# Optimization experiments

Hardware: AMD Instinct MI355X
Metric: run time of the kernel (lower is better)

## Reference

```python
import jax, jax.numpy as jnp
import numpy as np
import math

B, T, C, H = 2, 2048, 1024, 16
D = C // H  # head dim = 64

def setup_inputs() -> dict:
    key = jax.random.key(0)
    ks = jax.random.split(key, 5)
    scale_in = 1.0 / math.sqrt(C)
    x = jax.random.normal(ks[0], (B, T, C), dtype=jnp.float32)
    W_attn = jax.random.normal(ks[1], (C, 3 * C), dtype=jnp.float32) * scale_in
    b_attn = jnp.zeros((3 * C,), dtype=jnp.float32)
    W_proj = jax.random.normal(ks[2], (C, C), dtype=jnp.float32) * scale_in
    b_proj = jnp.zeros((C,), dtype=jnp.float32)
    return {"x": x, "W_attn": W_attn, "b_attn": b_attn, "W_proj": W_proj, "b_proj": b_proj}

def reference(x, W_attn, b_attn, W_proj, b_proj):
    qkv = x @ W_attn + b_attn                      # [B,T,3C]
    q, k, v = jnp.split(qkv, 3, axis=2)            # each [B,T,C]
    def heads(t):
        return t.reshape(B, T, H, D).transpose(0, 2, 1, 3)  # [B,H,T,D]
    q, k, v = heads(q), heads(k), heads(v)
    # NOTE: original scales by 1/sqrt(n_embd), not 1/sqrt(head_dim)
    scores = jnp.einsum('bhtd,bhsd->bhts', q, k) / math.sqrt(C)  # [B,H,T,T]
    mask = jnp.tril(jnp.ones((T, T), dtype=scores.dtype))
    scores = scores + (mask - 1.0) * 1e9
    attn = jax.nn.softmax(scores, axis=-1)
    out = jnp.einsum('bhts,bhsd->bhtd', attn, v)   # [B,H,T,D]
    out = out.transpose(0, 2, 1, 3).reshape(B, T, C)
    return out @ W_proj + b_proj
```

## Files before the change

kernel.cpp:

```cpp
#include <hip/hip_runtime.h>
#include <hip/hip_bf16.h>


typedef __attribute__((ext_vector_type(8))) short bf16x8;
typedef __attribute__((ext_vector_type(4))) short bf16x4;
typedef __attribute__((ext_vector_type(4))) float f32x4;

__device__ __forceinline__ short f2bs(float f) {
    union { __hip_bfloat16 h; short s; } u;
    u.h = __float2bfloat16(f);
    return u.s;
}

__device__ __forceinline__ short f2bs_trunc(float f) {
    return (short)(__float_as_uint(f) >> 16);
}

#define GLOAD_LDS16(gp, lp)                                                        \
    __builtin_amdgcn_global_load_lds((const __attribute__((address_space(1))) void*)(gp), \
                                     (__attribute__((address_space(3))) void*)(lp), 16, 0, 0)

__global__ __launch_bounds__(256) void convx(
    const float* __restrict__ X, short* __restrict__ Xb)
{
    const size_t i = ((size_t)blockIdx.x * 256 + threadIdx.x) * 8;
    float4 a = *(const float4*)(X + i);
    float4 b = *(const float4*)(X + i + 4);
    bf16x8 s;
    s[0] = f2bs(a.x); s[1] = f2bs(a.y); s[2] = f2bs(a.z); s[3] = f2bs(a.w);
    s[4] = f2bs(b.x); s[5] = f2bs(b.y); s[6] = f2bs(b.z); s[7] = f2bs(b.w);
    *(bf16x8*)(Xb + i) = s;
}

__global__ __launch_bounds__(256) void convt(
    const float* __restrict__ W, short* __restrict__ Wt, int K, int N)
{
    __shared__ short t[64 * 72];
    const int tid = threadIdx.x;
    const int n0 = blockIdx.x * 64, k0 = blockIdx.y * 64;
    #pragma unroll
    for (int i = 0; i < 4; i++) {
        int k = (tid >> 4) + i * 16;
        int n = (tid & 15) * 4;
        float4 v = *(const float4*)(W + (size_t)(k0 + k) * N + n0 + n);
        t[(n + 0) * 72 + k] = f2bs(v.x);
        t[(n + 1) * 72 + k] = f2bs(v.y);
        t[(n + 2) * 72 + k] = f2bs(v.z);
        t[(n + 3) * 72 + k] = f2bs(v.w);
    }
    __syncthreads();
    #pragma unroll
    for (int i = 0; i < 2; i++) {
        int n  = (tid >> 3) + i * 32;
        int kc = (tid & 7) * 8;
        bf16x8 v = *(const bf16x8*)&t[n * 72 + kc];
        *(bf16x8*)(Wt + (size_t)(n0 + n) * K + k0 + kc) = v;
    }
}

__global__ __launch_bounds__(512) void qkv_gemm(
    const short* __restrict__ Xb, const short* __restrict__ Wt,
    const float* __restrict__ bias,
    short* __restrict__ Qw, short* __restrict__ Kw, short* __restrict__ Vt)
{
    __shared__ short LB[40960];

    const int tid  = threadIdx.x;
    const int lane = tid & 63;
    const int wid  = tid >> 6;
    const int wm = wid >> 2, wn = wid & 3;
    const int g = lane >> 4, cc = lane & 15;
    const int sw = cc & 7;

    const int bid   = blockIdx.x;
    const int xcd   = bid & 7;
    const int r     = bid >> 3;
    const int m0 = ((xcd & 3) * 8 + (r & 7)) * 128;
    const int n0 = ((xcd >> 2) * 8 + (r >> 3)) * 192;

    f32x4 acc[4][3];
    const f32x4 z4 = {0.f, 0.f, 0.f, 0.f};
    #pragma unroll
    for (int i = 0; i < 4; i++)
        #pragma unroll
        for (int j = 0; j < 3; j++) acc[i][j] = z4;

    auto STAGE = [&](int t, int buf) {
        const int k0 = t * 64;
        short* Ab = LB + buf * 8192;
        short* Bb = LB + 16384 + buf * 12288;
        #pragma unroll
        for (int j = 0; j < 2; j++) {
            int c = j * 512 + tid;
            int row = c >> 3, sch = (c & 7) ^ (row & 7);
            GLOAD_LDS16(Xb + (size_t)(m0 + row) * 1024 + k0 + sch * 8, Ab + c * 8);
        }
        #pragma unroll
        for (int j = 0; j < 3; j++) {
            int c = j * 512 + tid;
            int row = c >> 3, sch = (c & 7) ^ (row & 7);
            GLOAD_LDS16(Wt + (size_t)(n0 + row) * 1024 + k0 + sch * 8, Bb + c * 8);
        }
    };

    STAGE(0, 0);
    STAGE(1, 1);
    asm volatile("s_waitcnt vmcnt(5)" ::: "memory");
    asm volatile("s_barrier" ::: "memory");

    const int NT = 16;
    for (int t = 0; t < NT; t++) {
        const short* Ab = LB + (t & 1) * 8192;
        const short* Bb = LB + 16384 + (t & 1) * 12288;

        bf16x8 bfr[3][2];
        #pragma unroll
        for (int nf = 0; nf < 3; nf++)
            #pragma unroll
            for (int kk = 0; kk < 2; kk++)
                bfr[nf][kk] = *(const bf16x8*)&Bb[(wn * 48 + nf * 16 + cc) * 64 +
                                                  ((kk * 4 + g) ^ sw) * 8];
        bf16x8 af[4][2];
        #pragma unroll
        for (int mf = 0; mf < 4; mf++)
            #pragma unroll
            for (int kk = 0; kk < 2; kk++)
                af[mf][kk] = *(const bf16x8*)&Ab[(wm * 64 + mf * 16 + cc) * 64 +
                                                 ((kk * 4 + g) ^ sw) * 8];
        __builtin_amdgcn_s_setprio(1);
        #pragma unroll
        for (int mf = 0; mf < 4; mf++)
            #pragma unroll
            for (int nf = 0; nf < 3; nf++)
                #pragma unroll
                for (int kk = 0; kk < 2; kk++)
                    acc[mf][nf] = __builtin_amdgcn_mfma_f32_16x16x32_bf16(
                        af[mf][kk], bfr[nf][kk], acc[mf][nf], 0, 0, 0);
        __builtin_amdgcn_s_setprio(0);

        asm volatile("s_barrier" ::: "memory");
        if (t + 2 < NT) {
            STAGE(t + 2, t & 1);
            asm volatile("s_waitcnt vmcnt(5)" ::: "memory");
            asm volatile("s_barrier" ::: "memory");
        } else if (t + 1 < NT) {
            asm volatile("s_waitcnt vmcnt(0)" ::: "memory");
            asm volatile("s_barrier" ::: "memory");
        }
    }

    const float QSCALE = 0.04508422976f;
    const int vs = (n0 > 2048) ? n0 : 2048;
    const int nV = n0 + 192 - vs;
    short* Vstage = LB;

    __syncthreads();

    #pragma unroll
    for (int nf = 0; nf < 3; nf++) {
        int col = n0 + wn * 48 + nf * 16 + cc;
        int which = col >> 10;
        int ci = col & 1023;
        int h = ci >> 6, d = ci & 63;
        float bv = bias[col];
        #pragma unroll
        for (int mf = 0; mf < 4; mf++) {
            if (which == 2) {
                int tl = wm * 64 + mf * 16 + g * 4;
                int pl = (tl & ~31) | (((tl >> 2) & 3) * 8 + ((tl >> 4) & 1) * 4);
                bf16x4 pk;
                #pragma unroll
                for (int r2 = 0; r2 < 4; r2++) pk[r2] = f2bs(acc[mf][nf][r2] + bv);
                *(bf16x4*)&Vstage[(col - vs) * 136 + pl] = pk;
            } else {
                #pragma unroll
                for (int r2 = 0; r2 < 4; r2++) {
                    int row = m0 + wm * 64 + mf * 16 + g * 4 + r2;
                    int b = row >> 11, tt = row & 2047;
                    int bh = b * 16 + h;
                    float v = acc[mf][nf][r2] + bv;
                    if (which == 0) Qw[((size_t)bh * 2048 + tt) * 64 + d] = f2bs(v * QSCALE);
                    else            Kw[((size_t)bh * 2048 + tt) * 64 + d] = f2bs(v);
                }
            }
        }
    }

    if (nV > 0) {
        __syncthreads();
        const int bb = m0 >> 11;
        const int tbase = m0 & 2047;
        const int total = nV * 16;
        for (int cidx = tid; cidx < total; cidx += 512) {
            int vc = cidx >> 4, toff = (cidx & 15) * 8;
            bf16x8 v = *(const bf16x8*)&Vstage[vc * 136 + toff];
            int col = vs + vc;
            int ci = col & 1023;
            int h2 = ci >> 6, d2 = ci & 63;
            *(bf16x8*)(Vt + ((size_t)(bb * 16 + h2) * 64 + d2) * 2048 + tbase + toff) = v;
        }
    }
}

__global__ __launch_bounds__(256) void attn_v16(
    const short* __restrict__ Qw, const short* __restrict__ Kw,
    const short* __restrict__ Vt, short* __restrict__ Aout)
{
    __shared__ short Klds[2][64 * 64];
    __shared__ short Vlds[2][64 * 64];
    const int tid  = threadIdx.x;
    const int lane = tid & 63;
    const int wid  = tid >> 6;
    const int g = lane >> 4, cc = lane & 15;
    const int bid = blockIdx.x;
    const int bh = bid & 31;
    const int grp = 31 - (bid >> 5);
    const int b = bh >> 4, h = bh & 15;
    const short* Qb = Qw + (size_t)bh * 2048 * 64;
    const short* Kb = Kw + (size_t)bh * 2048 * 64;
    const short* Vb = Vt + (size_t)bh * 64 * 2048;

    const f32x4 z4 = {0.f, 0.f, 0.f, 0.f};
    bf16x8 ones;
    #pragma unroll
    for (int i = 0; i < 8; i++) ones[i] = (short)0x3F80;

    auto STAGE = [&](int t, int buf) {
        const int kv0 = t * 64;
        #pragma unroll
        for (int j = 0; j < 2; j++) {
            int c = tid + j * 256;
            int row = c >> 3, sch = (c & 7) ^ (row & 7);
            GLOAD_LDS16(Kb + (size_t)(kv0 + row) * 64 + sch * 8, &Klds[buf][c * 8]);
            GLOAD_LDS16(Vb + (size_t)row * 2048 + kv0 + sch * 8, &Vlds[buf][c * 8]);
        }
    };

    const int q0 = grp * 64 + wid * 16;
    const int NT = grp + 1;

    bf16x8 qf0[2];
    #pragma unroll
    for (int ds = 0; ds < 2; ds++)
        qf0[ds] = *(const bf16x8*)(Qb + (q0 + cc) * 64 + ds * 32 + g * 8);

    f32x4 o[4], ol;
    #pragma unroll
    for (int ch = 0; ch < 4; ch++) o[ch] = z4;
    ol = z4;
    float m_r = -1e30f;

    STAGE(0, 0);
    STAGE((NT > 1) ? 1 : 0, 1);
    asm volatile("s_waitcnt vmcnt(4)" ::: "memory");
    asm volatile("s_barrier" ::: "memory");

    for (int t = 0; t < NT; t++) {
        const int kv0 = t * 64;
        const short* Kt = Klds[t & 1];
        const short* Vt_ = Vlds[t & 1];
        const bool masked = (t == NT - 1);

        bf16x8 kf[8];
        #pragma unroll
        for (int kvc = 0; kvc < 4; kvc++) {
            int row = kvc * 16 + cc;
            #pragma unroll
            for (int ds = 0; ds < 2; ds++)
                kf[kvc * 2 + ds] = *(const bf16x8*)&Kt[row * 64 +
                                                       (((ds * 4 + g) ^ (row & 7)) * 8)];
        }
        f32x4 s_[4];
        #pragma unroll
        for (int kvc = 0; kvc < 4; kvc++) {
            s_[kvc] = z4;
            #pragma unroll
            for (int ds = 0; ds < 2; ds++)
                s_[kvc] = __builtin_amdgcn_mfma_f32_16x16x32_bf16(
                    kf[kvc * 2 + ds], qf0[ds], s_[kvc], 0, 0, 0);
        }
        bf16x8 vf[8];
        #pragma unroll
        for (int kvh = 0; kvh < 2; kvh++)
            #pragma unroll
            for (int ch = 0; ch < 4; ch++) {
                int row = ch * 16 + cc;
                vf[kvh * 4 + ch] = *(const bf16x8*)&Vt_[row * 64 +
                                                        (((kvh * 4 + g) ^ (row & 7)) * 8)];
            }

        bf16x8 pb_[2];
        {
            float sv[16];
            #pragma unroll
            for (int kvc = 0; kvc < 4; kvc++)
                #pragma unroll
                for (int r = 0; r < 4; r++) {
                    float v = s_[kvc][r];
                    if (masked) {
                        int kv = kv0 + kvc * 16 + g * 4 + r;
                        v = (kv <= q0 + cc) ? v : -1e30f;
                    }
                    sv[kvc * 4 + r] = v;
                }
            float lm = sv[0];
            #pragma unroll
            for (int i = 1; i < 16; i++) lm = fmaxf(lm, sv[i]);
            if (__any(lm > m_r + 6.0f)) {
                float mx = fmaxf(lm, __shfl_xor(lm, 16));
                mx = fmaxf(mx, __shfl_xor(mx, 32));
                float mn = fmaxf(m_r, mx);
                float a = exp2f(m_r - mn);
                #pragma unroll
                for (int ch = 0; ch < 4; ch++)
                    #pragma unroll
                    for (int r = 0; r < 4; r++) o[ch][r] *= a;
                #pragma unroll
                for (int r = 0; r < 4; r++) ol[r] *= a;
                m_r = mn;
            }
            #pragma unroll
            for (int i = 0; i < 16; i++) {
                float p = exp2f(sv[i] - m_r);
                pb_[i >> 3][i & 7] = f2bs_trunc(p);
            }
        }
        #pragma unroll
        for (int kvh = 0; kvh < 2; kvh++) {
            #pragma unroll
            for (int ch = 0; ch < 4; ch++)
                o[ch] = __builtin_amdgcn_mfma_f32_16x16x32_bf16(
                    vf[kvh * 4 + ch], pb_[kvh], o[ch], 0, 0, 0);
            ol = __builtin_amdgcn_mfma_f32_16x16x32_bf16(ones, pb_[kvh], ol, 0, 0, 0);
        }

        asm volatile("s_barrier" ::: "memory");
        if (t + 2 < NT) {
            STAGE(t + 2, t & 1);
            asm volatile("s_waitcnt vmcnt(4)" ::: "memory");
            asm volatile("s_barrier" ::: "memory");
        } else if (t + 1 < NT) {
            asm volatile("s_waitcnt vmcnt(0)" ::: "memory");
            asm volatile("s_barrier" ::: "memory");
        }
    }

    const float rl = 1.0f / ol[0];
    const int t2 = q0 + cc;
    #pragma unroll
    for (int ch = 0; ch < 4; ch++) {
        bf16x4 ov;
        #pragma unroll
        for (int r = 0; r < 4; r++) ov[r] = f2bs(o[ch][r] * rl);
        *(bf16x4*)(Aout + ((size_t)b * 2048 + t2) * 1024 + h * 64 + ch * 16 + g * 4) = ov;
    }
}

__global__ __launch_bounds__(512) void proj_gemm(
    const short* __restrict__ A, const short* __restrict__ Wt,
    const float* __restrict__ bias, float* __restrict__ Out)
{
    __shared__ short Alds[2][256 * 64];
    __shared__ short Blds[2][64 * 64];
    const int tid  = threadIdx.x;
    const int lane = tid & 63;
    const int wid  = tid >> 6;
    const int wm = wid >> 1, wn = wid & 1;
    const int g = lane >> 4, cc = lane & 15;
    const int sw = cc & 7;

    const int bid  = blockIdx.x;
    const int wgid = (bid & 7) * 32 + (bid >> 3);
    const int n0 = (wgid >> 4) * 64;
    const int m0 = (wgid & 15) * 256;

    f32x4 acc[4][2];
    const f32x4 z4 = {0.f, 0.f, 0.f, 0.f};
    #pragma unroll
    for (int i = 0; i < 4; i++)
        #pragma unroll
        for (int j = 0; j < 2; j++) acc[i][j] = z4;

    auto STAGE = [&](int t, int buf) {
        const int k0 = t * 64;
        #pragma unroll
        for (int j = 0; j < 4; j++) {
            int c = j * 512 + wid * 64 + lane;
            int row = c >> 3, sch = (c & 7) ^ (row & 7);
            GLOAD_LDS16(A + (size_t)(m0 + row) * 1024 + k0 + sch * 8,
                        &Alds[buf][c * 8]);
        }
        {
            int c = wid * 64 + lane;
            int row = c >> 3, sch = (c & 7) ^ (row & 7);
            GLOAD_LDS16(Wt + (size_t)(n0 + row) * 1024 + k0 + sch * 8,
                        &Blds[buf][c * 8]);
        }
    };

    STAGE(0, 0);
    STAGE(1, 1);
    asm volatile("s_waitcnt vmcnt(5)" ::: "memory");
    asm volatile("s_barrier" ::: "memory");

    const int NT = 16;
    for (int t = 0; t < NT; t++) {
        const short* Ab = Alds[t & 1];
        const short* Bb = Blds[t & 1];

        bf16x8 bfr[2][2];
        #pragma unroll
        for (int nf = 0; nf < 2; nf++)
            #pragma unroll
            for (int kk = 0; kk < 2; kk++)
                bfr[nf][kk] = *(const bf16x8*)&Bb[(wn * 32 + nf * 16 + cc) * 64 +
                                                  ((kk * 4 + g) ^ sw) * 8];
        bf16x8 af[4][2];
        #pragma unroll
        for (int mf = 0; mf < 4; mf++)
            #pragma unroll
            for (int kk = 0; kk < 2; kk++)
                af[mf][kk] = *(const bf16x8*)&Ab[(wm * 64 + mf * 16 + cc) * 64 +
                                                 ((kk * 4 + g) ^ sw) * 8];
        __builtin_amdgcn_s_setprio(1);
        #pragma unroll
        for (int mf = 0; mf < 4; mf++)
            #pragma unroll
            for (int nf = 0; nf < 2; nf++)
                #pragma unroll
                for (int kk = 0; kk < 2; kk++)
                    acc[mf][nf] = __builtin_amdgcn_mfma_f32_16x16x32_bf16(
                        af[mf][kk], bfr[nf][kk], acc[mf][nf], 0, 0, 0);
        __builtin_amdgcn_s_setprio(0);

        asm volatile("s_barrier" ::: "memory");
        if (t + 2 < NT) {
            STAGE(t + 2, t & 1);
            asm volatile("s_waitcnt vmcnt(5)" ::: "memory");
            asm volatile("s_barrier" ::: "memory");
        } else if (t + 1 < NT) {
            asm volatile("s_waitcnt vmcnt(0)" ::: "memory");
            asm volatile("s_barrier" ::: "memory");
        }
    }

    #pragma unroll
    for (int nf = 0; nf < 2; nf++) {
        int col = n0 + wn * 32 + nf * 16 + cc;
        float bv = bias[col];
        #pragma unroll
        for (int mf = 0; mf < 4; mf++) {
            #pragma unroll
            for (int r = 0; r < 4; r++) {
                int row = m0 + wm * 64 + mf * 16 + g * 4 + r;
                Out[(size_t)row * 1024 + col] = acc[mf][nf][r] + bv;
            }
        }
    }
}

extern "C" void kernel_launch(void* const* d_in, const int* in_sizes, int n_in,
                              void* d_out, int out_size, void* d_ws, size_t ws_size,
                              hipStream_t stream)
{
    const float* x      = (const float*)d_in[0];
    const float* W_attn = (const float*)d_in[1];
    const float* b_attn = (const float*)d_in[2];
    const float* W_proj = (const float*)d_in[3];
    const float* b_proj = (const float*)d_in[4];
    float* out = (float*)d_out;

    const size_t SZ = (size_t)4096 * 1024;
    short* R1 = (short*)d_ws;
    short* Qw = R1 + SZ;
    short* Kw = Qw + SZ;
    short* Vt = Kw + SZ;

    short* Wt_attn = R1;
    short* Aout    = R1;
    short* Wt_proj = Qw;
    short* Xb      = (short*)d_out;

    convx<<<dim3(2048), 256, 0, stream>>>(x, Xb);
    convt<<<dim3(48, 16), 256, 0, stream>>>(W_attn, Wt_attn, 1024, 3072);
    qkv_gemm<<<dim3(512), 512, 0, stream>>>(Xb, Wt_attn, b_attn, Qw, Kw, Vt);
    attn_v16<<<dim3(1024), 256, 0, stream>>>(Qw, Kw, Vt, Aout);
    convt<<<dim3(16, 16), 256, 0, stream>>>(W_proj, Wt_proj, 1024, 1024);
    proj_gemm<<<dim3(256), 512, 0, stream>>>(Aout, Wt_proj, b_proj, out);
}
```

Measured before the change: 105.7 us.

## Process two 64-row query tiles per attention block to reuse K/V tiles

Each attention workgroup now handles 128 query rows (two 64-row sub-tiles A and B) instead of 64, so every K/V tile staged in LDS feeds both sub-tiles. The grid is halved to 512 blocks and the block-to-query-group mapping is reordered so the largest groups launch first. This cuts K/V global loads and LDS staging per unit of work. In exchange it raises register pressure from the doubled accumulators and query fragments, and lowers the block count, which may hurt occupancy and load balance.

```diff
diff --git a/kernel.cpp b/kernel.cpp
--- a/kernel.cpp
+++ b/kernel.cpp
@@ -202,7 +202,7 @@
     }
 }
 
-__global__ __launch_bounds__(256) void attn_v16(
+__global__ __launch_bounds__(256) void attn_v17(
     const short* __restrict__ Qw, const short* __restrict__ Kw,
     const short* __restrict__ Vt, short* __restrict__ Aout)
 {
@@ -214,7 +214,8 @@
     const int g = lane >> 4, cc = lane & 15;
     const int bid = blockIdx.x;
     const int bh = bid & 31;
-    const int grp = 31 - (bid >> 5);
+    const int gq = bid >> 5;
+    const int grp = (gq < 8) ? (15 - gq) : (gq - 8);
     const int b = bh >> 4, h = bh & 15;
     const short* Qb = Qw + (size_t)bh * 2048 * 64;
     const short* Kb = Kw + (size_t)bh * 2048 * 64;
@@ -236,22 +237,25 @@
         }
     };
 
-    const int q0 = grp * 64 + wid * 16;
-    const int NT = grp + 1;
-
-    bf16x8 qf0[2];
-    #pragma unroll
-    for (int ds = 0; ds < 2; ds++)
-        qf0[ds] = *(const bf16x8*)(Qb + (q0 + cc) * 64 + ds * 32 + g * 8);
-
-    f32x4 o[4], ol;
-    #pragma unroll
-    for (int ch = 0; ch < 4; ch++) o[ch] = z4;
-    ol = z4;
-    float m_r = -1e30f;
+    const int q0A = grp * 128 + wid * 16;
+    const int q0B = grp * 128 + 64 + wid * 16;
+    const int NT = 2 * grp + 2;
+
+    bf16x8 qfA[2], qfB[2];
+    #pragma unroll
+    for (int ds = 0; ds < 2; ds++) {
+        qfA[ds] = *(const bf16x8*)(Qb + (q0A + cc) * 64 + ds * 32 + g * 8);
+        qfB[ds] = *(const bf16x8*)(Qb + (q0B + cc) * 64 + ds * 32 + g * 8);
+    }
+
+    f32x4 oA[4], oB[4], olA, olB;
+    #pragma unroll
+    for (int ch = 0; ch < 4; ch++) { oA[ch] = z4; oB[ch] = z4; }
+    olA = z4; olB = z4;
+    float mA = -1e30f, mB = -1e30f;
 
     STAGE(0, 0);
-    STAGE((NT > 1) ? 1 : 0, 1);
+    STAGE(1, 1);
     asm volatile("s_waitcnt vmcnt(4)" ::: "memory");
     asm volatile("s_barrier" ::: "memory");
 
@@ -259,7 +263,9 @@
         const int kv0 = t * 64;
         const short* Kt = Klds[t & 1];
         const short* Vt_ = Vlds[t & 1];
-        const bool masked = (t == NT - 1);
+        const bool actA = (t < NT - 1);
+        const bool mskA = (t == NT - 2);
+        const bool mskB = (t == NT - 1);
 
         bf16x8 kf[8];
         #pragma unroll
@@ -270,14 +276,24 @@
                 kf[kvc * 2 + ds] = *(const bf16x8*)&Kt[row * 64 +
                                                        (((ds * 4 + g) ^ (row & 7)) * 8)];
         }
-        f32x4 s_[4];
+        f32x4 sA_[4], sB_[4];
         #pragma unroll
         for (int kvc = 0; kvc < 4; kvc++) {
-            s_[kvc] = z4;
+            sB_[kvc] = z4;
             #pragma unroll
             for (int ds = 0; ds < 2; ds++)
-                s_[kvc] = __builtin_amdgcn_mfma_f32_16x16x32_bf16(
-                    kf[kvc * 2 + ds], qf0[ds], s_[kvc], 0, 0, 0);
+                sB_[kvc] = __builtin_amdgcn_mfma_f32_16x16x32_bf16(
+                    kf[kvc * 2 + ds], qfB[ds], sB_[kvc], 0, 0, 0);
+        }
+        if (actA) {
+            #pragma unroll
+            for (int kvc = 0; kvc < 4; kvc++) {
+                sA_[kvc] = z4;
+                #pragma unroll
+                for (int ds = 0; ds < 2; ds++)
+                    sA_[kvc] = __builtin_amdgcn_mfma_f32_16x16x32_bf16(
+                        kf[kvc * 2 + ds], qfA[ds], sA_[kvc], 0, 0, 0);
+            }
         }
         bf16x8 vf[8];
         #pragma unroll
@@ -289,49 +305,96 @@
                                                         (((kvh * 4 + g) ^ (row & 7)) * 8)];
             }
 
-        bf16x8 pb_[2];
+        bf16x8 pbB[2];
         {
             float sv[16];
             #pragma unroll
             for (int kvc = 0; kvc < 4; kvc++)
                 #pragma unroll
                 for (int r = 0; r < 4; r++) {
-                    float v = s_[kvc][r];
-                    if (masked) {
+                    float v = sB_[kvc][r];
+                    if (mskB) {
                         int kv = kv0 + kvc * 16 + g * 4 + r;
-                        v = (kv <= q0 + cc) ? v : -1e30f;
+                        v = (kv <= q0B + cc) ? v : -1e30f;
                     }
                     sv[kvc * 4 + r] = v;
                 }
             float lm = sv[0];
             #pragma unroll
             for (int i = 1; i < 16; i++) lm = fmaxf(lm, sv[i]);
-            if (__any(lm > m_r + 6.0f)) {
+            if (__any(lm > mB + 6.0f)) {
                 float mx = fmaxf(lm, __shfl_xor(lm, 16));
                 mx = fmaxf(mx, __shfl_xor(mx, 32));
-                float mn = fmaxf(m_r, mx);
-                float a = exp2f(m_r - mn);
+                float mn = fmaxf(mB, mx);
+                float a = exp2f(mB - mn);
                 #pragma unroll
                 for (int ch = 0; ch < 4; ch++)
                     #pragma unroll
-                    for (int r = 0; r < 4; r++) o[ch][r] *= a;
-                #pragma unroll
-                for (int r = 0; r < 4; r++) ol[r] *= a;
-                m_r = mn;
+                    for (int r = 0; r < 4; r++) oB[ch][r] *= a;
+                #pragma unroll
+                for (int r = 0; r < 4; r++) olB[r] *= a;
+                mB = mn;
             }
             #pragma unroll
             for (int i = 0; i < 16; i++) {
-                float p = exp2f(sv[i] - m_r);
-                pb_[i >> 3][i & 7] = f2bs_trunc(p);
-            }
-        }
+                float p = exp2f(sv[i] - mB);
+                pbB[i >> 3][i & 7] = f2bs_trunc(p);
+            }
+        }
+        bf16x8 pbA[2];
+        if (actA) {
+            float sv[16];
+            #pragma unroll
+            for (int kvc = 0; kvc < 4; kvc++)
+                #pragma unroll
+                for (int r = 0; r < 4; r++) {
+                    float v = sA_[kvc][r];
+                    if (mskA) {
+                        int kv = kv0 + kvc * 16 + g * 4 + r;
+                        v = (kv <= q0A + cc) ? v : -1e30f;
+                    }
+                    sv[kvc * 4 + r] = v;
+                }
+            float lm = sv[0];
+            #pragma unroll
+            for (int i = 1; i < 16; i++) lm = fmaxf(lm, sv[i]);
+            if (__any(lm > mA + 6.0f)) {
+                float mx = fmaxf(lm, __shfl_xor(lm, 16));
+                mx = fmaxf(mx, __shfl_xor(mx, 32));
+                float mn = fmaxf(mA, mx);
+                float a = exp2f(mA - mn);
+                #pragma unroll
+                for (int ch = 0; ch < 4; ch++)
+                    #pragma unroll
+                    for (int r = 0; r < 4; r++) oA[ch][r] *= a;
+                #pragma unroll
+                for (int r = 0; r < 4; r++) olA[r] *= a;
+                mA = mn;
+            }
+            #pragma unroll
+            for (int i = 0; i < 16; i++) {
+                float p = exp2f(sv[i] - mA);
+                pbA[i >> 3][i & 7] = f2bs_trunc(p);
+            }
+        }
+
         #pragma unroll
         for (int kvh = 0; kvh < 2; kvh++) {
             #pragma unroll
             for (int ch = 0; ch < 4; ch++)
-                o[ch] = __builtin_amdgcn_mfma_f32_16x16x32_bf16(
-                    vf[kvh * 4 + ch], pb_[kvh], o[ch], 0, 0, 0);
-            ol = __builtin_amdgcn_mfma_f32_16x16x32_bf16(ones, pb_[kvh], ol, 0, 0, 0);
+                oB[ch] = __builtin_amdgcn_mfma_f32_16x16x32_bf16(
+                    vf[kvh * 4 + ch], pbB[kvh], oB[ch], 0, 0, 0);
+            olB = __builtin_amdgcn_mfma_f32_16x16x32_bf16(ones, pbB[kvh], olB, 0, 0, 0);
+        }
+        if (actA) {
+            #pragma unroll
+            for (int kvh = 0; kvh < 2; kvh++) {
+                #pragma unroll
+                for (int ch = 0; ch < 4; ch++)
+                    oA[ch] = __builtin_amdgcn_mfma_f32_16x16x32_bf16(
+                        vf[kvh * 4 + ch], pbA[kvh], oA[ch], 0, 0, 0);
+                olA = __builtin_amdgcn_mfma_f32_16x16x32_bf16(ones, pbA[kvh], olA, 0, 0, 0);
+            }
         }
 
         asm volatile("s_barrier" ::: "memory");
@@ -345,14 +408,27 @@
         }
     }
 
-    const float rl = 1.0f / ol[0];
-    const int t2 = q0 + cc;
-    #pragma unroll
-    for (int ch = 0; ch < 4; ch++) {
-        bf16x4 ov;
-        #pragma unroll
-        for (int r = 0; r < 4; r++) ov[r] = f2bs(o[ch][r] * rl);
-        *(bf16x4*)(Aout + ((size_t)b * 2048 + t2) * 1024 + h * 64 + ch * 16 + g * 4) = ov;
+    {
+        const float rl = 1.0f / olA[0];
+        const int t2 = q0A + cc;
+        #pragma unroll
+        for (int ch = 0; ch < 4; ch++) {
+            bf16x4 ov;
+            #pragma unroll
+            for (int r = 0; r < 4; r++) ov[r] = f2bs(oA[ch][r] * rl);
+            *(bf16x4*)(Aout + ((size_t)b * 2048 + t2) * 1024 + h * 64 + ch * 16 + g * 4) = ov;
+        }
+    }
+    {
+        const float rl = 1.0f / olB[0];
+        const int t2 = q0B + cc;
+        #pragma unroll
+        for (int ch = 0; ch < 4; ch++) {
+            bf16x4 ov;
+            #pragma unroll
+            for (int r = 0; r < 4; r++) ov[r] = f2bs(oB[ch][r] * rl);
+            *(bf16x4*)(Aout + ((size_t)b * 2048 + t2) * 1024 + h * 64 + ch * 16 + g * 4) = ov;
+        }
     }
 }
 
@@ -484,7 +560,7 @@
     convx<<<dim3(2048), 256, 0, stream>>>(x, Xb);
     convt<<<dim3(48, 16), 256, 0, stream>>>(W_attn, Wt_attn, 1024, 3072);
     qkv_gemm<<<dim3(512), 512, 0, stream>>>(Xb, Wt_attn, b_attn, Qw, Kw, Vt);
-    attn_v16<<<dim3(1024), 256, 0, stream>>>(Qw, Kw, Vt, Aout);
+    attn_v17<<<dim3(512), 256, 0, stream>>>(Qw, Kw, Vt, Aout);
     convt<<<dim3(16, 16), 256, 0, stream>>>(W_proj, Wt_proj, 1024, 1024);
     proj_gemm<<<dim3(256), 512, 0, stream>>>(Aout, Wt_proj, b_proj, out);
 }
```

New measurement: 122.7 us. 16.1% more time.
